# Performance work log

Measured on AMD Instinct MI355X. Metric: run time of the kernel, lower is better.

The kernel has to match this reference:

```python
import jax, jax.numpy as jnp
import numpy as np

HEAD_DIM = 64

def setup_inputs() -> dict:
    key = jax.random.key(0)
    k1, k2, k3, k4, k5 = jax.random.split(key, 5)
    T, B, E = 2048, 4, 1024
    KD = 64  # kdim
    x = jax.random.normal(k1, (T, B, E), dtype=jnp.float32)
    in_proj_weight = jax.random.normal(k2, (3 * KD, HEAD_DIM), dtype=jnp.float32) * (1.0 / np.sqrt(HEAD_DIM))
    in_proj_bias = jnp.zeros((3 * KD,), dtype=jnp.float32)
    out_w = jax.random.normal(k4, (HEAD_DIM, KD), dtype=jnp.float32) * (1.0 / np.sqrt(KD))
    out_b = jnp.zeros((HEAD_DIM,), dtype=jnp.float32)
    return {"x": x, "in_proj_weight": in_proj_weight, "in_proj_bias": in_proj_bias,
            "out_w": out_w, "out_b": out_b}

def reference(x, in_proj_weight, in_proj_bias, out_w, out_b):
    # x: [T, B, E] with E = H * HEAD_DIM (qkv_same self-attention path)
    T, B, E = x.shape
    H = E // HEAD_DIM
    KD = in_proj_weight.shape[0] // 3
    scaling = HEAD_DIM ** (-0.5)
    # reshape splits embed dim into heads: [T, B*H, 64]
    xh = x.reshape(T, B * H, HEAD_DIM)
    # fused in-projection: [T, B*H, 3*KD], then chunk into q/k/v
    qkv = xh @ in_proj_weight.T + in_proj_bias
    q, k, v = jnp.split(qkv, 3, axis=-1)          # each [T, B*H, KD]
    q = q * scaling
    q = q.transpose(1, 0, 2)                      # [B*H, T, KD]
    k = k.transpose(1, 0, 2)
    v = v.transpose(1, 0, 2)
    scores = jnp.einsum('btd,bsd->bts', q, k)     # [B*H, T, T]
    w = jax.nn.softmax(scores, axis=-1)
    attn = jnp.einsum('bts,bsd->btd', w, v)       # [B*H, T, KD]
    attn = attn.transpose(1, 0, 2).reshape(T, B, H, KD)
    out = attn @ out_w.T + out_b                  # [T, B, H, HEAD_DIM]
    out = out.reshape(T, B, H * HEAD_DIM)         # [T, B, E]
    # averaged attention weights over heads: [B, T, T]
    avg_w = w.reshape(B, H, T, T).sum(axis=1) / H
    return out, avg_w
```

## Files before the change

### kernel.cpp

```cpp
#include <hip/hip_runtime.h>
#include <hip/hip_bf16.h>

#define T_DIM 2048
#define B_DIM 4
#define E_DIM 1024

typedef __bf16 bf16_t;
typedef bf16_t bf16x8 __attribute__((ext_vector_type(8)));
typedef float f32x4 __attribute__((ext_vector_type(4)));
typedef float f32x16 __attribute__((ext_vector_type(16)));

union frag_u { uint4 u; bf16x8 b; };

constexpr float SCALEQ = 0.18033688011112042f;

__device__ __forceinline__ f32x16 mfma32(bf16x8 a, bf16x8 b, f32x16 c) {
  return __builtin_amdgcn_mfma_f32_32x32x16_bf16(a, b, c, 0, 0, 0);
}
__device__ __forceinline__ unsigned packbf(float a, float b) {
  union { bf16_t h[2]; unsigned u; } r;
  r.h[0] = (bf16_t)a; r.h[1] = (bf16_t)b; return r.u;
}
__device__ __forceinline__ void pl32swap(unsigned &x, unsigned &y) {
  asm volatile("v_permlane32_swap_b32 %0, %1" : "+v"(x), "+v"(y));
}
__device__ __forceinline__ void gload16(const void* g, void* l) {
  __builtin_amdgcn_global_load_lds((const __attribute__((address_space(1))) void*)g,
                                   (__attribute__((address_space(3))) void*)l, 16, 0, 0);
}
__device__ __forceinline__ float ex2(float x) { return __builtin_amdgcn_exp2f(x); }

#define VMCNT4 do { asm volatile("s_waitcnt vmcnt(4)" ::: "memory"); \
                    __builtin_amdgcn_sched_barrier(0); } while (0)
#define VMCNT0 do { asm volatile("s_waitcnt vmcnt(0)" ::: "memory"); \
                    __builtin_amdgcn_sched_barrier(0); } while (0)
#define LGKM0  do { asm volatile("s_waitcnt lgkmcnt(0)" ::: "memory"); \
                    __builtin_amdgcn_sched_barrier(0); } while (0)
#define SBAR   do { __builtin_amdgcn_s_barrier(); \
                    __builtin_amdgcn_sched_barrier(0); } while (0)

template <int O>
__device__ __forceinline__ uint4 mkfrag(const f32x16& A) {
  unsigned X = packbf(A[O + 0], A[O + 1]);
  unsigned Z = packbf(A[O + 2], A[O + 3]);
  unsigned Y = packbf(A[O + 4], A[O + 5]);
  unsigned W = packbf(A[O + 6], A[O + 7]);
  pl32swap(X, Y); pl32swap(Z, W);
  return (uint4){X, Z, Y, W};
}

__device__ __forceinline__ float tree16(const f32x16& v) {
  float a0 = v[0] + v[1],   a1 = v[2] + v[3];
  float a2 = v[4] + v[5],   a3 = v[6] + v[7];
  float a4 = v[8] + v[9],   a5 = v[10] + v[11];
  float a6 = v[12] + v[13], a7 = v[14] + v[15];
  float b0 = a0 + a1, b1 = a2 + a3, b2 = a4 + a5, b3 = a6 + a7;
  return (b0 + b1) + (b2 + b3);
}

__global__ __launch_bounds__(256) void qkv_kernel(
    const float* __restrict__ x, const float* __restrict__ W,
    const float* __restrict__ bias,
    bf16_t* __restrict__ Qc, bf16_t* __restrict__ Kc, bf16_t* __restrict__ Vc) {
  __shared__ __align__(16) char xlds[16384];
  __shared__ __align__(16) char wlds[24576];
  __shared__ float bs[192];
  const int tid = threadIdx.x;
  const int bh = blockIdx.x >> 4;
  const int tt = blockIdx.x & 15;
  const int b = bh >> 4, h = bh & 15;
  const int t0 = tt * 128;
  const int wid = tid >> 6, lane = tid & 63;
  const int lq = lane & 31, hi = lane >> 5;

  for (int i = tid; i < 1024; i += 256) {
    int t = i >> 3, oct = i & 7;
    const float* src = x + ((size_t)(t0 + t) * B_DIM + b) * E_DIM + h * 64 + oct * 8;
    float4 f0 = *(const float4*)src;
    float4 f1 = *(const float4*)(src + 4);
    uint4 u;
    u.x = packbf(f0.x, f0.y); u.y = packbf(f0.z, f0.w);
    u.z = packbf(f1.x, f1.y); u.w = packbf(f1.z, f1.w);
    *(uint4*)(xlds + oct * 2048 + t * 16) = u;
  }
  for (int i = tid; i < 1536; i += 256) {
    int r = i >> 3, oct = i & 7;
    const float* src = W + r * 64 + oct * 8;
    float4 f0 = *(const float4*)src;
    float4 f1 = *(const float4*)(src + 4);
    uint4 u;
    u.x = packbf(f0.x, f0.y); u.y = packbf(f0.z, f0.w);
    u.z = packbf(f1.x, f1.y); u.w = packbf(f1.z, f1.w);
    *(uint4*)(wlds + oct * 3072 + r * 16) = u;
  }
  if (tid < 192) bs[tid] = bias[tid];
  __syncthreads();

  frag_u bx[4];
  #pragma unroll
  for (int s = 0; s < 4; ++s)
    bx[s].u = *(const uint4*)(xlds + (s * 2 + hi) * 2048 + (wid * 32 + lq) * 16);

  f32x16 acc[6];
  #pragma unroll
  for (int mt = 0; mt < 6; ++mt)
    #pragma unroll
    for (int r = 0; r < 16; ++r) acc[mt][r] = 0.f;

  #pragma unroll
  for (int mt = 0; mt < 6; ++mt) {
    #pragma unroll
    for (int s = 0; s < 4; ++s) {
      frag_u aw;
      aw.u = *(const uint4*)(wlds + (s * 2 + hi) * 3072 + (mt * 32 + lq) * 16);
      acc[mt] = mfma32(aw.b, bx[s].b, acc[mt]);
    }
  }

  const size_t tb = ((size_t)bh * 32 + (t0 >> 6) + (wid >> 1)) * 4096;
  const int trow = (wid & 1) * 32 + lq;

  #pragma unroll
  for (int mt = 0; mt < 6; ++mt) {
    #pragma unroll
    for (int g = 0; g < 4; ++g) {
      int rbase = mt * 32 + 8 * g + 4 * hi;
      float4 bq = *(const float4*)&bs[rbase];
      float v0 = acc[mt][4 * g + 0] + bq.x;
      float v1 = acc[mt][4 * g + 1] + bq.y;
      float v2 = acc[mt][4 * g + 2] + bq.z;
      float v3 = acc[mt][4 * g + 3] + bq.w;
      if (mt < 2) {
        union { ushort4 us; unsigned u2[2]; } pk;
        pk.u2[0] = packbf(v0 * SCALEQ, v1 * SCALEQ);
        pk.u2[1] = packbf(v2 * SCALEQ, v3 * SCALEQ);
        int d0 = rbase;
        *(ushort4*)(Qc + tb + (d0 >> 3) * 512 + trow * 8 + (d0 & 7)) = pk.us;
      } else if (mt < 4) {
        union { ushort4 us; unsigned u2[2]; } pk;
        pk.u2[0] = packbf(v0, v1);
        pk.u2[1] = packbf(v2, v3);
        int d0 = rbase - 64;
        *(ushort4*)(Kc + tb + (d0 >> 3) * 512 + trow * 8 + (d0 & 7)) = pk.us;
      } else {
        int d0 = rbase - 128;
        bf16_t* vdst = Vc + tb + (trow >> 3) * 512 + (trow & 7);
        vdst[(size_t)(d0 + 0) * 8] = (bf16_t)v0;
        vdst[(size_t)(d0 + 1) * 8] = (bf16_t)v1;
        vdst[(size_t)(d0 + 2) * 8] = (bf16_t)v2;
        vdst[(size_t)(d0 + 3) * 8] = (bf16_t)v3;
      }
    }
  }
}

__global__ __launch_bounds__(256, 2) void flash_kernel(
    const bf16_t* __restrict__ Qc, const bf16_t* __restrict__ Kc,
    const bf16_t* __restrict__ Vc,
    const float* __restrict__ Wo, const float* __restrict__ bo,
    float* __restrict__ out, float* __restrict__ Lv) {
  const int tid = threadIdx.x;
  const int bh = blockIdx.x & 63;
  const int qb = blockIdx.x >> 6;
  const int b = bh >> 4, h = bh & 15;
  const int wid = tid >> 6, lane = tid & 63;
  const int lq = lane & 31, hi = lane >> 5;
  const int qw = qb * 256 + wid * 64;
  const int rot = ((wid * 8) + ((qb & 1) * 4)) & 31;

  const bf16_t* qtb = Qc + ((size_t)bh * 32 + (qw >> 6)) * 4096;
  frag_u qfA[4], qfB[4];
  #pragma unroll
  for (int s = 0; s < 4; ++s) {
    qfA[s].u = *(const uint4*)(qtb + (s * 2 + hi) * 512 + lq * 8);
    qfB[s].u = *(const uint4*)(qtb + (s * 2 + hi) * 512 + (32 + lq) * 8);
  }

  f32x16 zc;
  #pragma unroll
  for (int i = 0; i < 16; ++i) zc[i] = 0.f;

  f32x16 oA0, oA1, oB0, oB1;
  #pragma unroll
  for (int i = 0; i < 16; ++i) { oA0[i] = 0.f; oA1[i] = 0.f; oB0[i] = 0.f; oB1[i] = 0.f; }
  float lAacc = 0.f, lBacc = 0.f;

  const bf16_t* kbh = Kc + (size_t)bh * 131072;
  const bf16_t* vbh = Vc + (size_t)bh * 131072;

  for (int ti = 0; ti < 32; ++ti) {
    const int t = (ti + rot) & 31;
    const bf16_t* kt = kbh + (size_t)t * 4096;
    const bf16_t* vt = vbh + (size_t)t * 4096;

    bf16x8 k0[4], k1[4], v0[4], v1[4];
    #pragma unroll
    for (int s = 0; s < 4; ++s) {
      frag_u f0, f1, g0, g1;
      f0.u = *(const uint4*)(kt + (s * 2 + hi) * 512 + lq * 8);
      f1.u = *(const uint4*)(kt + (s * 2 + hi) * 512 + (32 + lq) * 8);
      g0.u = *(const uint4*)(vt + (s * 2 + hi) * 512 + lq * 8);
      g1.u = *(const uint4*)(vt + (s * 2 + hi) * 512 + (32 + lq) * 8);
      k0[s] = f0.b; k1[s] = f1.b; v0[s] = g0.b; v1[s] = g1.b;
    }

    f32x16 aA0, aA1, aB0, aB1;
    __builtin_amdgcn_s_setprio(1);
    aA0 = mfma32(k0[0], qfA[0].b, zc);
    aA1 = mfma32(k1[0], qfA[0].b, zc);
    aB0 = mfma32(k0[0], qfB[0].b, zc);
    aB1 = mfma32(k1[0], qfB[0].b, zc);
    #pragma unroll
    for (int s = 1; s < 4; ++s) {
      aA0 = mfma32(k0[s], qfA[s].b, aA0);
      aA1 = mfma32(k1[s], qfA[s].b, aA1);
      aB0 = mfma32(k0[s], qfB[s].b, aB0);
      aB1 = mfma32(k1[s], qfB[s].b, aB1);
    }
    __builtin_amdgcn_s_setprio(0);

    #pragma unroll
    for (int i = 0; i < 16; ++i) {
      aA0[i] = ex2(aA0[i]); aA1[i] = ex2(aA1[i]);
      aB0[i] = ex2(aB0[i]); aB1[i] = ex2(aB1[i]);
    }
    lAacc += tree16(aA0 + aA1);
    lBacc += tree16(aB0 + aB1);

    frag_u pA0, pA1, pA2, pA3, pB0, pB1, pB2, pB3;
    pA0.u = mkfrag<0>(aA0); pA1.u = mkfrag<8>(aA0);
    pA2.u = mkfrag<0>(aA1); pA3.u = mkfrag<8>(aA1);
    pB0.u = mkfrag<0>(aB0); pB1.u = mkfrag<8>(aB0);
    pB2.u = mkfrag<0>(aB1); pB3.u = mkfrag<8>(aB1);

    __builtin_amdgcn_s_setprio(1);
    oA0 = mfma32(v0[0], pA0.b, oA0); oA1 = mfma32(v1[0], pA0.b, oA1);
    oB0 = mfma32(v0[0], pB0.b, oB0); oB1 = mfma32(v1[0], pB0.b, oB1);
    oA0 = mfma32(v0[1], pA1.b, oA0); oA1 = mfma32(v1[1], pA1.b, oA1);
    oB0 = mfma32(v0[1], pB1.b, oB0); oB1 = mfma32(v1[1], pB1.b, oB1);
    oA0 = mfma32(v0[2], pA2.b, oA0); oA1 = mfma32(v1[2], pA2.b, oA1);
    oB0 = mfma32(v0[2], pB2.b, oB0); oB1 = mfma32(v1[2], pB2.b, oB1);
    oA0 = mfma32(v0[3], pA3.b, oA0); oA1 = mfma32(v1[3], pA3.b, oA1);
    oB0 = mfma32(v0[3], pB3.b, oB0); oB1 = mfma32(v1[3], pB3.b, oB1);
    __builtin_amdgcn_s_setprio(0);
  }

  float ltA = lAacc + __shfl_xor(lAacc, 32);
  float ltB = lBacc + __shfl_xor(lBacc, 32);
  float iA = 1.f / ltA, iB = 1.f / ltB;
  #pragma unroll
  for (int i = 0; i < 16; ++i) { oA0[i] *= iA; oA1[i] *= iA; oB0[i] *= iB; oB1[i] *= iB; }

  frag_u fA[4], fB[4];
  fA[0].u = mkfrag<0>(oA0); fA[1].u = mkfrag<8>(oA0);
  fA[2].u = mkfrag<0>(oA1); fA[3].u = mkfrag<8>(oA1);
  fB[0].u = mkfrag<0>(oB0); fB[1].u = mkfrag<8>(oB0);
  fB[2].u = mkfrag<0>(oB1); fB[3].u = mkfrag<8>(oB1);

  f32x16 cA0, cA1, cB0, cB1;
  #pragma unroll
  for (int i = 0; i < 16; ++i) { cA0[i] = 0.f; cA1[i] = 0.f; cB0[i] = 0.f; cB1[i] = 0.f; }
  #pragma unroll
  for (int s = 0; s < 4; ++s) {
    frag_u w0, w1;
    {
      const float* ws0 = Wo + lq * 64 + (s * 2 + hi) * 8;
      float4 a = *(const float4*)ws0;
      float4 c = *(const float4*)(ws0 + 4);
      w0.u = (uint4){packbf(a.x, a.y), packbf(a.z, a.w),
                     packbf(c.x, c.y), packbf(c.z, c.w)};
      const float* ws1 = Wo + (32 + lq) * 64 + (s * 2 + hi) * 8;
      float4 d = *(const float4*)ws1;
      float4 e = *(const float4*)(ws1 + 4);
      w1.u = (uint4){packbf(d.x, d.y), packbf(d.z, d.w),
                     packbf(e.x, e.y), packbf(e.z, e.w)};
    }
    cA0 = mfma32(fA[s].b, w0.b, cA0);
    cA1 = mfma32(fA[s].b, w1.b, cA1);
    cB0 = mfma32(fB[s].b, w0.b, cB0);
    cB1 = mfma32(fB[s].b, w1.b, cB1);
  }
  float bo0 = bo[lq], bo1 = bo[32 + lq];
  #pragma unroll
  for (int r = 0; r < 16; ++r) {
    int trA = qw + (r & 3) + 8 * (r >> 2) + 4 * hi;
    int trB = trA + 32;
    out[((size_t)trA * B_DIM + b) * E_DIM + h * 64 + lq]      = cA0[r] + bo0;
    out[((size_t)trA * B_DIM + b) * E_DIM + h * 64 + 32 + lq] = cA1[r] + bo1;
    out[((size_t)trB * B_DIM + b) * E_DIM + h * 64 + lq]      = cB0[r] + bo0;
    out[((size_t)trB * B_DIM + b) * E_DIM + h * 64 + 32 + lq] = cB1[r] + bo1;
  }
  if (lane < 32) {
    Lv[(size_t)bh * T_DIM + qw + lq] = ltA;
    Lv[(size_t)bh * T_DIM + qw + 32 + lq] = ltB;
  }
}

__global__ __launch_bounds__(512, 2) void avgw_kernel(
    const bf16_t* __restrict__ Qc, const bf16_t* __restrict__ Kc,
    const float* __restrict__ Lv, float* __restrict__ avgw) {
  __shared__ __align__(16) char qlds[2][16384];
  __shared__ __align__(16) char klds[2][16384];
  __shared__ float lw[16][128];
  const int tid = threadIdx.x;
  const int bid = ((blockIdx.x & 7) << 7) | (blockIdx.x >> 3);
  const int b = bid >> 8, tq = (bid >> 4) & 15, sq = bid & 15;
  const int t0 = tq * 128, s0 = sq * 128;
  const int wid = tid >> 6, lane = tid & 63;
  const int lq = lane & 31, hi = lane >> 5;
  const int wr = wid >> 2, wc = wid & 3;

  for (int i = tid; i < 2048; i += 512) {
    int h = i >> 7, tt = i & 127;
    size_t idx = ((size_t)(b * 16 + h)) * T_DIM + t0 + tt;
    lw[h][tt] = 1.0f / (16.0f * Lv[idx]);
  }

  auto stage = [&](int buf, int h) {
    int bh = b * 16 + h;
    const bf16_t* qt = Qc + ((size_t)bh * 32 + (t0 >> 6)) * 4096;
    const bf16_t* kt = Kc + ((size_t)bh * 32 + (s0 >> 6)) * 4096;
    #pragma unroll
    for (int j = 0; j < 2; ++j) {
      gload16(qt + wid * 1024 + j * 512 + lane * 8, qlds[buf] + wid * 2048 + j * 1024);
      gload16(kt + wid * 1024 + j * 512 + lane * 8, klds[buf] + wid * 2048 + j * 1024);
    }
  };

  f32x16 zc;
  #pragma unroll
  for (int r = 0; r < 16; ++r) zc[r] = 0.f;

  f32x16 sacc[2];
  #pragma unroll
  for (int i = 0; i < 2; ++i)
    #pragma unroll
    for (int r = 0; r < 16; ++r) sacc[i][r] = 0.f;

  stage(0, 0); stage(1, 1);
  VMCNT4; LGKM0;
  SBAR;

  for (int h = 0; h < 16; ++h) {
    const char* qb = qlds[h & 1];
    const char* kb = klds[h & 1];

    frag_u aq[2][4], ak[4];
    #pragma unroll
    for (int s = 0; s < 4; ++s) {
      int rk = wc * 32 + lq;
      ak[s].u = *(const uint4*)(kb + (rk >> 6) * 8192 + (s * 2 + hi) * 1024 + (rk & 63) * 16);
      #pragma unroll
      for (int i = 0; i < 2; ++i) {
        int rq = wr * 64 + i * 32 + lq;
        aq[i][s].u = *(const uint4*)(qb + (rq >> 6) * 8192 + (s * 2 + hi) * 1024 + (rq & 63) * 16);
      }
    }
    LGKM0;
    SBAR;
    if (h + 2 < 16) stage(h & 1, h + 2);

    #pragma unroll
    for (int i = 0; i < 2; ++i) {
      __builtin_amdgcn_s_setprio(1);
      f32x16 c = mfma32(aq[i][0].b, ak[0].b, zc);
      #pragma unroll
      for (int s = 1; s < 4; ++s) c = mfma32(aq[i][s].b, ak[s].b, c);
      __builtin_amdgcn_s_setprio(0);
      #pragma unroll
      for (int g = 0; g < 4; ++g) {
        f32x4 l4 = *(const f32x4*)&lw[h][wr * 64 + i * 32 + 8 * g + 4 * hi];
        #pragma unroll
        for (int e = 0; e < 4; ++e)
          sacc[i][4 * g + e] += ex2(c[4 * g + e]) * l4[e];
      }
    }

    if (h < 14) { VMCNT4; } else { VMCNT0; }
    SBAR;
  }

  #pragma unroll
  for (int i = 0; i < 2; ++i)
    #pragma unroll
    for (int r = 0; r < 16; ++r) {
      int trow = t0 + wr * 64 + i * 32 + (r & 3) + ((r >> 2) << 3) + (hi << 2);
      int scol = s0 + wc * 32 + lq;
      avgw[((size_t)b * T_DIM + trow) * T_DIM + scol] = sacc[i][r];
    }
}

extern "C" void kernel_launch(void* const* d_in, const int* in_sizes, int n_in,
                              void* d_out, int out_size, void* d_ws, size_t ws_size,
                              hipStream_t stream) {
  const float* x    = (const float*)d_in[0];
  const float* W    = (const float*)d_in[1];
  const float* bias = (const float*)d_in[2];
  const float* Wo   = (const float*)d_in[3];
  const float* bo   = (const float*)d_in[4];
  float* out  = (float*)d_out;
  float* avgw = out + (size_t)T_DIM * B_DIM * E_DIM;

  char* ws = (char*)d_ws;
  bf16_t* Qc = (bf16_t*)(ws);
  bf16_t* Kc = (bf16_t*)(ws + (16u << 20));
  bf16_t* Vc = (bf16_t*)(ws + (32u << 20));
  float*  Lv = (float*)(ws + (48u << 20));

  qkv_kernel<<<dim3(1024), dim3(256), 0, stream>>>(x, W, bias, Qc, Kc, Vc);
  flash_kernel<<<dim3(512), dim3(256), 0, stream>>>(Qc, Kc, Vc, Wo, bo, out, Lv);
  avgw_kernel<<<dim3(1024), dim3(512), 0, stream>>>(Qc, Kc, Lv, avgw);
}
```

Measured before the change: 176.2 us.

## Split flash attention key range across waves and simplify avgw pipelining

```diff
diff --git a/kernel.cpp b/kernel.cpp
--- a/kernel.cpp
+++ b/kernel.cpp
@@ -29,15 +29,6 @@
                                    (__attribute__((address_space(3))) void*)l, 16, 0, 0);
 }
 __device__ __forceinline__ float ex2(float x) { return __builtin_amdgcn_exp2f(x); }
-
-#define VMCNT4 do { asm volatile("s_waitcnt vmcnt(4)" ::: "memory"); \
-                    __builtin_amdgcn_sched_barrier(0); } while (0)
-#define VMCNT0 do { asm volatile("s_waitcnt vmcnt(0)" ::: "memory"); \
-                    __builtin_amdgcn_sched_barrier(0); } while (0)
-#define LGKM0  do { asm volatile("s_waitcnt lgkmcnt(0)" ::: "memory"); \
-                    __builtin_amdgcn_sched_barrier(0); } while (0)
-#define SBAR   do { __builtin_amdgcn_s_barrier(); \
-                    __builtin_amdgcn_sched_barrier(0); } while (0)
 
 template <int O>
 __device__ __forceinline__ uint4 mkfrag(const f32x16& A) {
@@ -154,19 +145,21 @@
   }
 }
 
-__global__ __launch_bounds__(256, 2) void flash_kernel(
+__global__ __launch_bounds__(256, 4) void flash_kernel(
     const bf16_t* __restrict__ Qc, const bf16_t* __restrict__ Kc,
     const bf16_t* __restrict__ Vc,
     const float* __restrict__ Wo, const float* __restrict__ bo,
     float* __restrict__ out, float* __restrict__ Lv) {
+  __shared__ __align__(16) char cbuf[32768];
+  __shared__ float lbuf[128];
   const int tid = threadIdx.x;
   const int bh = blockIdx.x & 63;
-  const int qb = blockIdx.x >> 6;
+  const int qblk = blockIdx.x >> 6;
   const int b = bh >> 4, h = bh & 15;
   const int wid = tid >> 6, lane = tid & 63;
   const int lq = lane & 31, hi = lane >> 5;
-  const int qw = qb * 256 + wid * 64;
-  const int rot = ((wid * 8) + ((qb & 1) * 4)) & 31;
+  const int qt = wid >> 1, kh = wid & 1;
+  const int qw = qblk * 128 + qt * 64;
 
   const bf16_t* qtb = Qc + ((size_t)bh * 32 + (qw >> 6)) * 4096;
   frag_u qfA[4], qfB[4];
@@ -188,8 +181,8 @@
   const bf16_t* kbh = Kc + (size_t)bh * 131072;
   const bf16_t* vbh = Vc + (size_t)bh * 131072;
 
-  for (int ti = 0; ti < 32; ++ti) {
-    const int t = (ti + rot) & 31;
+  for (int ti = 0; ti < 16; ++ti) {
+    const int t = kh * 16 + ti;
     const bf16_t* kt = kbh + (size_t)t * 4096;
     const bf16_t* vt = vbh + (size_t)t * 4096;
 
@@ -247,6 +240,48 @@
 
   float ltA = lAacc + __shfl_xor(lAacc, 32);
   float ltB = lBacc + __shfl_xor(lBacc, 32);
+
+  if (kh == 1) {
+    char* myr = cbuf + qt * 16384 + lane * 256;
+    #pragma unroll
+    for (int g = 0; g < 4; ++g) {
+      f32x4 w0, w1, w2, w3;
+      #pragma unroll
+      for (int e = 0; e < 4; ++e) {
+        w0[e] = oA0[4 * g + e]; w1[e] = oA1[4 * g + e];
+        w2[e] = oB0[4 * g + e]; w3[e] = oB1[4 * g + e];
+      }
+      *(f32x4*)(myr + (((g)      ^ (lane & 15)) * 16)) = w0;
+      *(f32x4*)(myr + (((4 + g)  ^ (lane & 15)) * 16)) = w1;
+      *(f32x4*)(myr + (((8 + g)  ^ (lane & 15)) * 16)) = w2;
+      *(f32x4*)(myr + (((12 + g) ^ (lane & 15)) * 16)) = w3;
+    }
+    if (lane < 32) {
+      lbuf[qt * 64 + lq] = ltA;
+      lbuf[qt * 64 + 32 + lq] = ltB;
+    }
+  }
+  __syncthreads();
+  if (kh == 1) return;
+
+  {
+    const char* pr = cbuf + qt * 16384 + lane * 256;
+    #pragma unroll
+    for (int g = 0; g < 4; ++g) {
+      f32x4 w0 = *(const f32x4*)(pr + (((g)      ^ (lane & 15)) * 16));
+      f32x4 w1 = *(const f32x4*)(pr + (((4 + g)  ^ (lane & 15)) * 16));
+      f32x4 w2 = *(const f32x4*)(pr + (((8 + g)  ^ (lane & 15)) * 16));
+      f32x4 w3 = *(const f32x4*)(pr + (((12 + g) ^ (lane & 15)) * 16));
+      #pragma unroll
+      for (int e = 0; e < 4; ++e) {
+        oA0[4 * g + e] += w0[e]; oA1[4 * g + e] += w1[e];
+        oB0[4 * g + e] += w2[e]; oB1[4 * g + e] += w3[e];
+      }
+    }
+    ltA += lbuf[qt * 64 + lq];
+    ltB += lbuf[qt * 64 + 32 + lq];
+  }
+
   float iA = 1.f / ltA, iB = 1.f / ltB;
   #pragma unroll
   for (int i = 0; i < 16; ++i) { oA0[i] *= iA; oA1[i] *= iA; oB0[i] *= iB; oB1[i] *= iB; }
@@ -337,11 +372,11 @@
     #pragma unroll
     for (int r = 0; r < 16; ++r) sacc[i][r] = 0.f;
 
-  stage(0, 0); stage(1, 1);
-  VMCNT4; LGKM0;
-  SBAR;
+  stage(0, 0);
+  __syncthreads();
 
   for (int h = 0; h < 16; ++h) {
+    if (h < 15) stage((h + 1) & 1, h + 1);
     const char* qb = qlds[h & 1];
     const char* kb = klds[h & 1];
 
@@ -356,9 +391,6 @@
         aq[i][s].u = *(const uint4*)(qb + (rq >> 6) * 8192 + (s * 2 + hi) * 1024 + (rq & 63) * 16);
       }
     }
-    LGKM0;
-    SBAR;
-    if (h + 2 < 16) stage(h & 1, h + 2);
 
     #pragma unroll
     for (int i = 0; i < 2; ++i) {
@@ -375,9 +407,7 @@
           sacc[i][4 * g + e] += ex2(c[4 * g + e]) * l4[e];
       }
     }
-
-    if (h < 14) { VMCNT4; } else { VMCNT0; }
-    SBAR;
+    __syncthreads();
   }
 
   #pragma unroll
@@ -408,6 +438,6 @@
   float*  Lv = (float*)(ws + (48u << 20));
 
   qkv_kernel<<<dim3(1024), dim3(256), 0, stream>>>(x, W, bias, Qc, Kc, Vc);
-  flash_kernel<<<dim3(512), dim3(256), 0, stream>>>(Qc, Kc, Vc, Wo, bo, out, Lv);
+  flash_kernel<<<dim3(1024), dim3(256), 0, stream>>>(Qc, Kc, Vc, Wo, bo, out, Lv);
   avgw_kernel<<<dim3(1024), dim3(512), 0, stream>>>(Qc, Kc, Lv, avgw);
 }
```

Result: slower. 626.6 us (+255.6%).
